# Kernel tuning notes

Hardware: AMD Instinct MI355X
Metric: run time of the kernel (lower is better)

## Reference

```python
import jax, jax.numpy as jnp
import numpy as np

EMBED_DIM = 1024
ATTN_DIM = 1024


def setup_inputs() -> dict:
    key = jax.random.key(0)
    k1, k2, k3, k4 = jax.random.split(key, 4)
    scale = 1.0 / np.sqrt(EMBED_DIM)
    return {
        "embedded": jax.random.normal(k1, (4, 2048, EMBED_DIM), dtype=jnp.float32),
        # weights stored as [in, out] (torch Linear applies x @ W.T)
        "Wk": jax.random.uniform(k2, (EMBED_DIM, ATTN_DIM), dtype=jnp.float32, minval=-scale, maxval=scale),
        "Wq": jax.random.uniform(k3, (EMBED_DIM, ATTN_DIM), dtype=jnp.float32, minval=-scale, maxval=scale),
        "Wv": jax.random.uniform(k4, (EMBED_DIM, ATTN_DIM), dtype=jnp.float32, minval=-scale, maxval=scale),
    }


def reference(embedded, Wk, Wq, Wv):
    b, t, _ = embedded.shape
    k = embedded @ Wk  # [b, t, d]
    q = embedded @ Wq
    v = embedded @ Wv
    scores = jnp.einsum("btd,bsd->bts", q, k) / jnp.sqrt(jnp.float32(k.shape[-1]))
    causal = jnp.tril(jnp.ones((t, t), dtype=bool))  # [t, t]
    scores = jnp.where(causal, scores, -jnp.inf)
    w = jax.nn.softmax(scores, axis=-1)
    o = jnp.einsum("bts,bsd->btd", w, v)
    return jnp.round(o * 10000.0) / 10000.0
```

## Files before the change

### kernel.cpp

```cpp
#include <hip/hip_runtime.h>
#include <cmath>

typedef _Float16 half8 __attribute__((ext_vector_type(8)));
typedef _Float16 half4 __attribute__((ext_vector_type(4)));
typedef float floatx4 __attribute__((ext_vector_type(4)));

__device__ __forceinline__ void load_lds16(const void* g, void* l) {
  __builtin_amdgcn_global_load_lds((const __attribute__((address_space(1))) void*)g,
                                   (__attribute__((address_space(3))) void*)l, 16, 0, 0);
}

__device__ __forceinline__ unsigned lds_addr(const void* p) {
  return (unsigned)(unsigned long long)(const __attribute__((address_space(3))) void*)p;
}

__device__ __forceinline__ half8 ds_read128(unsigned addr) {
  half8 r;
  asm volatile("ds_read_b128 %0, %1" : "=v"(r) : "v"(addr));
  return r;
}


__global__ void prep_kernel(const float* __restrict__ emb, const float* __restrict__ Wq,
                            const float* __restrict__ Wk, const float* __restrict__ Wv,
                            _Float16* __restrict__ Xp, _Float16* __restrict__ Wqp,
                            _Float16* __restrict__ Wkp, _Float16* __restrict__ Wvtp) {
  int p = blockIdx.x;
  if (p < 640) {
    __shared__ _Float16 lds[16 * 1032];
    const float* src;
    _Float16* dst;
    if (p < 512)      { src = emb + (size_t)p * 16384;        dst = Xp  + (size_t)p * 16384; }
    else if (p < 576) { src = Wq + (size_t)(p - 512) * 16384; dst = Wqp + (size_t)(p - 512) * 16384; }
    else              { src = Wk + (size_t)(p - 576) * 16384; dst = Wkp + (size_t)(p - 576) * 16384; }
    for (int it = 0; it < 16; ++it) {
      int idx = it * 256 + threadIdx.x;
      int row = idx >> 8, c4 = idx & 255;
      float4 v = ((const float4*)src)[row * 256 + c4];
      half4 h;
      h[0] = (_Float16)v.x; h[1] = (_Float16)v.y; h[2] = (_Float16)v.z; h[3] = (_Float16)v.w;
      *(half4*)(lds + row * 1032 + c4 * 4) = h;
    }
    __syncthreads();
    for (int it = 0; it < 8; ++it) {
      int c = it * 256 + threadIdx.x;
      int kb = c >> 6, k16 = (c >> 4) & 3, r = c & 15;
      half8 h = *(const half8*)(lds + r * 1032 + kb * 32 + k16 * 8);
      *(half8*)(dst + (size_t)c * 8) = h;
    }
  } else {
    __shared__ float tile[32][33];
    int q = p - 640;
    int n0 = (q & 31) * 32, k0 = (q >> 5) * 32;
    int c = threadIdx.x & 31, r8 = threadIdx.x >> 5;
    for (int pp = 0; pp < 4; ++pp) {
      int r = pp * 8 + r8;
      tile[r][c] = Wv[(size_t)(k0 + r) * 1024 + n0 + c];
    }
    __syncthreads();
    if (threadIdx.x < 128) {
      int rr = threadIdx.x & 31;
      int k16 = (threadIdx.x >> 5) & 3;
      half8 h;
      for (int kk = 0; kk < 8; ++kk) h[kk] = (_Float16)tile[k16 * 8 + kk][rr];
      int n_row = n0 + rr;
      size_t chunk = ((size_t)(n_row >> 4) * 32 + (k0 >> 5)) * 64 + (k16 << 4) + (n_row & 15);
      *(half8*)(Wvtp + chunk * 8) = h;
    }
  }
}

__device__ __forceinline__ void gemm_core(const _Float16* __restrict__ Ap, int kbA, int tA0,
                                          const _Float16* __restrict__ Bp, int kbB, int tB0,
                                          int kIters, _Float16* sA, _Float16* sB,
                                          floatx4 acc[4][4]) {
  int tid = threadIdx.x;
  int lane = tid & 63, wave = tid >> 6;
  int wm = (wave >> 1) << 6, wn = (wave & 1) << 6;
  const _Float16* gA0 = Ap + ((size_t)(tA0 + 2 * wave) * kbA) * 512 + lane * 8;
  const _Float16* gA1 = Ap + ((size_t)(tA0 + 2 * wave + 1) * kbA) * 512 + lane * 8;
  const _Float16* gB0 = Bp + ((size_t)(tB0 + 2 * wave) * kbB) * 512 + lane * 8;
  const _Float16* gB1 = Bp + ((size_t)(tB0 + 2 * wave + 1) * kbB) * 512 + lane * 8;
  int ta = wm >> 4, tb = wn >> 4, lo = lane * 8;
  int wo = wave * 1024;

  load_lds16(gA0, sA + wo);
  load_lds16(gA1, sA + wo + 512);
  load_lds16(gB0, sB + wo);
  load_lds16(gB1, sB + wo + 512);
  __syncthreads();

  int cur = 0;
  for (int kt = 0; kt < kIters; ++kt) {
    if (kt + 1 < kIters) {
      size_t kb = (size_t)(kt + 1) * 512;
      int nx = (cur ^ 1) << 12;
      load_lds16(gA0 + kb, sA + nx + wo);
      load_lds16(gA1 + kb, sA + nx + wo + 512);
      load_lds16(gB0 + kb, sB + nx + wo);
      load_lds16(gB1 + kb, sB + nx + wo + 512);
    }
    const _Float16* cA = sA + (cur << 12);
    const _Float16* cB = sB + (cur << 12);
    half8 af[4], bf[4];
    for (int i = 0; i < 4; ++i) af[i] = *(const half8*)(cA + (ta + i) * 512 + lo);
    for (int j = 0; j < 4; ++j) bf[j] = *(const half8*)(cB + (tb + j) * 512 + lo);
    __builtin_amdgcn_s_setprio(1);
    for (int i = 0; i < 4; ++i)
      for (int j = 0; j < 4; ++j)
        acc[i][j] = __builtin_amdgcn_mfma_f32_16x16x32_f16(af[i], bf[j], acc[i][j], 0, 0, 0);
    __builtin_amdgcn_s_setprio(0);
    if (kt + 1 < kIters) {
      __syncthreads();
      cur ^= 1;
    }
  }
}

__global__ void mt_kernel(const _Float16* __restrict__ Wkp, const _Float16* __restrict__ Wqp,
                          _Float16* __restrict__ Mtp) {
  __shared__ __align__(16) _Float16 sA[8192];
  __shared__ __align__(16) _Float16 sB[8192];
  floatx4 acc[4][4];
  for (int i = 0; i < 4; ++i)
    for (int j = 0; j < 4; ++j) acc[i][j] = (floatx4){0.f, 0.f, 0.f, 0.f};
  int m0 = blockIdx.y * 128, n0 = blockIdx.x * 128;
  gemm_core(Wkp, 32, m0 >> 4, Wqp, 32, n0 >> 4, 32, sA, sB, acc);
  int lane = threadIdx.x & 63, wave = threadIdx.x >> 6;
  int wm = (wave >> 1) << 6, wn = (wave & 1) << 6;
  int quad = lane >> 4, cl = lane & 15;
  for (int i = 0; i < 4; ++i)
    for (int j = 0; j < 4; ++j)
      for (int rr = 0; rr < 4; ++rr) {
        int row = m0 + wm + i * 16 + quad * 4 + rr;
        int col = n0 + wn + j * 16 + cl;
        size_t chunk = ((size_t)(row >> 4) * 32 + (col >> 5)) * 64 + (((col >> 3) & 3) << 4) + (row & 15);
        Mtp[chunk * 8 + (col & 7)] = (_Float16)acc[i][j][rr];
      }
}

#define NT_PROJ 16

__global__ __launch_bounds__(512, 2) void proj256_kernel(
    const _Float16* __restrict__ Ap, const _Float16* __restrict__ Bp,
    _Float16* __restrict__ XMp, _Float16* __restrict__ Vtp) {
  __shared__ __align__(16) _Float16 sh[65536];
  int tid = threadIdx.x;
  int lane = tid & 63, w = tid >> 6;
  int wr = w >> 2, wc = w & 3;
  int orig = blockIdx.x;
  int tile = (orig & 7) * 32 + (orig >> 3);
  int mtile = tile >> 3, ntile = tile & 7;
  int tA0 = mtile * 16, tB0 = ntile * 16;

  const _Float16* gB[4];
  int ldsB[4];
  for (int i = 0; i < 4; ++i) {
    int cb = w * 4 + i, pc = cb >> 1, kb = cb & 1;
    gB[i] = Bp + ((size_t)(tB0 + pc) * 32 + kb) * 512 + lane * 8;
    ldsB[i] = 16384 + cb * 512;
  }
  const _Float16* gA[4];
  int ldsA[4];
  {
    int kbw = w & 1, pihi = (w >> 2) * 8, pilo = (w >> 1) & 1;
    for (int q = 0; q < 4; ++q) {
      int p = 2 * q + pilo + pihi;
      gA[q] = Ap + ((size_t)(tA0 + p) * 32 + kbw) * 512 + lane * 8;
      ldsA[q] = (p * 2 + kbw) * 512;
    }
  }

  unsigned L = lds_addr(sh);
  unsigned baseA = L + (unsigned)(wr * 16384 + lane * 16);
  unsigned baseB = L + 32768u + (unsigned)(wc * 8192 + lane * 16);

  floatx4 acc[8][4];
  for (int m = 0; m < 8; ++m)
    for (int n = 0; n < 4; ++n) acc[m][n] = (floatx4){0.f, 0.f, 0.f, 0.f};

  for (int tt = 0; tt < 2; ++tt) {
    int bo = tt << 15;
    for (int i = 0; i < 4; ++i) load_lds16(gB[i] + (size_t)tt * 1024, sh + bo + ldsB[i]);
    for (int q = 0; q < 4; ++q) load_lds16(gA[q] + (size_t)tt * 1024, sh + bo + ldsA[q]);
  }
  asm volatile("s_waitcnt vmcnt(8)" ::: "memory");
  __builtin_amdgcn_s_barrier();

  half8 bf[4][2];
#pragma unroll 2
  for (int t = 0; t < NT_PROJ; ++t) {
    int bo = (t & 1) << 15;
    unsigned bob = (unsigned)(t & 1) << 16;
    unsigned aA = baseA + bob, aB = baseB + bob;
#pragma unroll
    for (int q = 0; q < 4; ++q) {
      half8 af[2][2];
      if (q == 0) {
        for (int n = 0; n < 4; ++n)
          for (int kb = 0; kb < 2; ++kb)
            bf[n][kb] = ds_read128(aB + (unsigned)(n * 2048 + kb * 1024));
      }
      for (int mm = 0; mm < 2; ++mm)
        for (int kb = 0; kb < 2; ++kb)
          af[mm][kb] = ds_read128(aA + (unsigned)((2 * q + mm) * 2048 + kb * 1024));
      if (q == 0) {
        if (t >= 1 && t + 1 < NT_PROJ)
          load_lds16(gA[3] + (size_t)(t + 1) * 1024, sh + (bo ^ 32768) + ldsA[3]);
      } else if (q == 1) {
        if (t + 2 < NT_PROJ)
          for (int i = 0; i < 4; ++i)
            load_lds16(gB[i] + (size_t)(t + 2) * 1024, sh + bo + ldsB[i]);
      } else if (q == 2) {
        if (t + 2 < NT_PROJ) {
          load_lds16(gA[0] + (size_t)(t + 2) * 1024, sh + bo + ldsA[0]);
          load_lds16(gA[1] + (size_t)(t + 2) * 1024, sh + bo + ldsA[1]);
        }
      } else {
        if (t < NT_PROJ - 1) {
          if (t + 2 < NT_PROJ) asm volatile("s_waitcnt vmcnt(6)" ::: "memory");
          else                 asm volatile("s_waitcnt vmcnt(0)" ::: "memory");
        }
        if (t + 2 < NT_PROJ)
          load_lds16(gA[2] + (size_t)(t + 2) * 1024, sh + bo + ldsA[2]);
      }
      __builtin_amdgcn_s_barrier();
      asm volatile("s_waitcnt lgkmcnt(0)" ::: "memory");
      __builtin_amdgcn_sched_barrier(0);
      __builtin_amdgcn_s_setprio(1);
      for (int mm = 0; mm < 2; ++mm)
        for (int n = 0; n < 4; ++n)
          for (int kb = 0; kb < 2; ++kb)
            acc[2 * q + mm][n] =
                __builtin_amdgcn_mfma_f32_16x16x32_f16(af[mm][kb], bf[n][kb], acc[2 * q + mm][n], 0, 0, 0);
      __builtin_amdgcn_s_setprio(0);
      __builtin_amdgcn_sched_barrier(0);
      __builtin_amdgcn_s_barrier();
    }
  }

  int quad = lane >> 4, cl = lane & 15;
  int which = ntile >> 2;
  for (int m = 0; m < 8; ++m)
    for (int n = 0; n < 4; ++n)
      for (int rr = 0; rr < 4; ++rr) {
        int rl = wr * 128 + m * 16 + quad * 4 + rr;
        int cg = wc * 64 + n * 16 + cl;
        _Float16 val = (_Float16)acc[m][n][rr];
        int lh;
        if (which) {
          lh = (((cg >> 4) * 8 + (rl >> 5)) << 9) + (((rl >> 3) & 3) << 7) + ((cg & 15) << 3) + (rl & 7);
        } else {
          lh = (((rl >> 4) * 8 + (cg >> 5)) << 9) + (((cg >> 3) & 3) << 7) + ((rl & 15) << 3) + (cg & 7);
        }
        sh[lh] = val;
      }
  __syncthreads();
  int b = mtile >> 3;
  if (which) {
    _Float16* dst = Vtp + (size_t)b * 2097152;
    for (int p = 0; p < 16; ++p) {
      size_t GB = (((size_t)(ntile & 3) * 16 + p) * 64 + (mtile & 7) * 8) * 512;
      *(half8*)(dst + GB + tid * 8) = *(const half8*)(sh + p * 4096 + tid * 8);
    }
  } else {
    _Float16* dst = XMp + (size_t)b * 2097152;
    for (int p = 0; p < 16; ++p) {
      size_t GB = (((size_t)(mtile & 7) * 16 + p) * 32 + (ntile & 3) * 8) * 512;
      *(half8*)(dst + GB + tid * 8) = *(const half8*)(sh + p * 4096 + tid * 8);
    }
  }
}

__global__ void qke_kernel(const _Float16* __restrict__ XMp, const _Float16* __restrict__ Xp,
                           _Float16* __restrict__ E, float* __restrict__ lsum) {
  __shared__ __align__(16) _Float16 sh[16384];
  int x = blockIdx.x, b = blockIdx.y;
  int p = (x & 7) * 17 + (x >> 3);
  int ti = 0;
  while ((ti + 1) * (ti + 2) / 2 <= p) ++ti;
  int tj = p - ti * (ti + 1) / 2;
  const _Float16* Ab = XMp + (size_t)b * 2097152;
  const _Float16* Bb = Xp + (size_t)b * 2097152;
  _Float16* Eb = E + (size_t)b * 4194304;
  floatx4 acc[4][4];
  for (int i = 0; i < 4; ++i)
    for (int j = 0; j < 4; ++j) acc[i][j] = (floatx4){0.f, 0.f, 0.f, 0.f};
  gemm_core(Ab, 32, ti * 8, Bb, 32, tj * 8, 32, sh, sh + 8192, acc);
  int lane = threadIdx.x & 63, wave = threadIdx.x >> 6;
  int wm = (wave >> 1) << 6, wn = (wave & 1) << 6;
  int quad = lane >> 4, cl = lane & 15;
  float rs[4][4];
  for (int i = 0; i < 4; ++i)
    for (int rr = 0; rr < 4; ++rr) rs[i][rr] = 0.f;
  __syncthreads();
  for (int i = 0; i < 4; ++i)
    for (int j = 0; j < 4; ++j)
      for (int rr = 0; rr < 4; ++rr) {
        int rl = wm + i * 16 + quad * 4 + rr;
        int cg = wn + j * 16 + cl;
        int row = ti * 128 + rl, col = tj * 128 + cg;
        float e = 0.f;
        if (col <= row) e = __expf(acc[i][j][rr] * 0.03125f - 12.0f);
        _Float16 eh = (_Float16)e;
        rs[i][rr] += (float)eh;
        int lh = (((rl >> 4) * 4 + (cg >> 5)) << 9) + (((cg >> 3) & 3) << 7) + ((rl & 15) << 3) + (cg & 7);
        sh[lh] = eh;
      }
  __syncthreads();
  for (int pp = 0; pp < 8; ++pp) {
    size_t GB = ((size_t)(ti * 8 + pp) * 64 + tj * 4) * 512;
    *(half8*)(Eb + GB + threadIdx.x * 8) = *(const half8*)(sh + pp * 2048 + threadIdx.x * 8);
  }
  float* lb = lsum + (size_t)b * 2048;
  for (int i = 0; i < 4; ++i)
    for (int rr = 0; rr < 4; ++rr) {
      float v = rs[i][rr];
      v += __shfl_xor(v, 1, 64);
      v += __shfl_xor(v, 2, 64);
      v += __shfl_xor(v, 4, 64);
      v += __shfl_xor(v, 8, 64);
      if (cl == 0) atomicAdd(lb + ti * 128 + wm + i * 16 + quad * 4 + rr, v);
    }
}

__global__ void pv_kernel(const _Float16* __restrict__ E, const _Float16* __restrict__ Vtp,
                          const float* __restrict__ lsum, float* __restrict__ out) {
  __shared__ __align__(16) _Float16 sA[8192];
  __shared__ __align__(16) _Float16 sB[8192];
  int orig = blockIdx.x + 8 * (blockIdx.y + 16 * blockIdx.z);
  int logical = (orig & 7) * 64 + (orig >> 3);
  int n0 = (logical & 7) * 128;
  int rest = logical >> 3;
  int y = rest & 15, b = rest >> 4;
  int ti = (y & 1) ? (15 - (y >> 1)) : (y >> 1);
  const _Float16* Pb = E + (size_t)b * 4194304;
  const _Float16* Vb = Vtp + (size_t)b * 2097152;
  floatx4 acc[4][4];
  for (int i = 0; i < 4; ++i)
    for (int j = 0; j < 4; ++j) acc[i][j] = (floatx4){0.f, 0.f, 0.f, 0.f};
  gemm_core(Pb, 64, ti * 8, Vb, 64, n0 >> 4, (ti + 1) * 4, sA, sB, acc);
  int lane = threadIdx.x & 63, wave = threadIdx.x >> 6;
  int wm = (wave >> 1) << 6, wn = (wave & 1) << 6;
  int quad = lane >> 4, cl = lane & 15;
  const float* lb = lsum + (size_t)b * 2048;
  for (int i = 0; i < 4; ++i)
    for (int rr = 0; rr < 4; ++rr) {
      int row = ti * 128 + wm + i * 16 + quad * 4 + rr;
      float inv = 1.0f / lb[row];
      for (int j = 0; j < 4; ++j) {
        int col = n0 + wn + j * 16 + cl;
        float v = acc[i][j][rr] * inv;
        out[((size_t)b * 2048 + row) * 1024 + col] = rintf(v * 10000.f) * 1e-4f;
      }
    }
}

extern "C" void kernel_launch(void* const* d_in, const int* in_sizes, int n_in,
                              void* d_out, int out_size, void* d_ws, size_t ws_size,
                              hipStream_t stream) {
  const float* emb = (const float*)d_in[0];
  const float* Wk = (const float*)d_in[1];
  const float* Wq = (const float*)d_in[2];
  const float* Wv = (const float*)d_in[3];
  float* out = (float*)d_out;

  _Float16* ws = (_Float16*)d_ws;
  _Float16* Xp   = ws;
  _Float16* Wqp  = Xp + (size_t)8192 * 1024;
  _Float16* Wkp  = Wqp + (size_t)1024 * 1024;
  _Float16* Mtp  = Wkp + (size_t)1024 * 1024;
  _Float16* Wvtp = Mtp + (size_t)1024 * 1024;
  _Float16* XMp  = Wvtp + (size_t)1024 * 1024;
  _Float16* Vtp  = XMp + (size_t)8192 * 1024;
  _Float16* Ebuf = Vtp + (size_t)8192 * 1024;
  float* lsum    = (float*)(Ebuf + (size_t)16 * 1024 * 1024);

  hipMemsetAsync(lsum, 0, 4 * 2048 * sizeof(float), stream);
  prep_kernel<<<1664, 256, 0, stream>>>(emb, Wq, Wk, Wv, Xp, Wqp, Wkp, Wvtp);
  mt_kernel<<<dim3(8, 8), 256, 0, stream>>>(Wkp, Wqp, Mtp);
  proj256_kernel<<<256, 512, 0, stream>>>(Xp, Mtp, XMp, Vtp);
  qke_kernel<<<dim3(136, 4), 256, 0, stream>>>(XMp, Xp, Ebuf, lsum);
  pv_kernel<<<dim3(8, 16, 4), 256, 0, stream>>>(Ebuf, Vtp, lsum, out);
}
```

Measured before the change: 223.3 us.

## Swizzle projection epilogue LDS, drop a barrier, vectorize PV output stores

```diff
diff --git a/kernel.cpp b/kernel.cpp
--- a/kernel.cpp
+++ b/kernel.cpp
@@ -18,6 +18,10 @@
   half8 r;
   asm volatile("ds_read_b128 %0, %1" : "=v"(r) : "v"(addr));
   return r;
+}
+
+__device__ __forceinline__ unsigned mswz(unsigned a) {
+  return a ^ (((a >> 7) & 1u) << 3) ^ (((a >> 6) & 1u) << 4);
 }
 
 
@@ -224,7 +228,6 @@
         if (t + 2 < NT_PROJ)
           load_lds16(gA[2] + (size_t)(t + 2) * 1024, sh + bo + ldsA[2]);
       }
-      __builtin_amdgcn_s_barrier();
       asm volatile("s_waitcnt lgkmcnt(0)" ::: "memory");
       __builtin_amdgcn_sched_barrier(0);
       __builtin_amdgcn_s_setprio(1);
@@ -247,13 +250,13 @@
         int rl = wr * 128 + m * 16 + quad * 4 + rr;
         int cg = wc * 64 + n * 16 + cl;
         _Float16 val = (_Float16)acc[m][n][rr];
-        int lh;
+        unsigned lh;
         if (which) {
-          lh = (((cg >> 4) * 8 + (rl >> 5)) << 9) + (((rl >> 3) & 3) << 7) + ((cg & 15) << 3) + (rl & 7);
+          lh = (((unsigned)(cg >> 4) * 8 + (rl >> 5)) << 9) + (((rl >> 3) & 3) << 7) + ((cg & 15) << 3) + (rl & 7);
         } else {
-          lh = (((rl >> 4) * 8 + (cg >> 5)) << 9) + (((cg >> 3) & 3) << 7) + ((rl & 15) << 3) + (cg & 7);
+          lh = (((unsigned)(rl >> 4) * 8 + (cg >> 5)) << 9) + (((cg >> 3) & 3) << 7) + ((rl & 15) << 3) + (cg & 7);
         }
-        sh[lh] = val;
+        sh[mswz(lh)] = val;
       }
   __syncthreads();
   int b = mtile >> 3;
@@ -261,13 +264,13 @@
     _Float16* dst = Vtp + (size_t)b * 2097152;
     for (int p = 0; p < 16; ++p) {
       size_t GB = (((size_t)(ntile & 3) * 16 + p) * 64 + (mtile & 7) * 8) * 512;
-      *(half8*)(dst + GB + tid * 8) = *(const half8*)(sh + p * 4096 + tid * 8);
+      *(half8*)(dst + GB + tid * 8) = *(const half8*)(sh + mswz((unsigned)(p * 4096 + tid * 8)));
     }
   } else {
     _Float16* dst = XMp + (size_t)b * 2097152;
     for (int p = 0; p < 16; ++p) {
       size_t GB = (((size_t)(mtile & 7) * 16 + p) * 32 + (ntile & 3) * 8) * 512;
-      *(half8*)(dst + GB + tid * 8) = *(const half8*)(sh + p * 4096 + tid * 8);
+      *(half8*)(dst + GB + tid * 8) = *(const half8*)(sh + mswz((unsigned)(p * 4096 + tid * 8)));
     }
   }
 }
@@ -339,21 +342,25 @@
   floatx4 acc[4][4];
   for (int i = 0; i < 4; ++i)
     for (int j = 0; j < 4; ++j) acc[i][j] = (floatx4){0.f, 0.f, 0.f, 0.f};
-  gemm_core(Pb, 64, ti * 8, Vb, 64, n0 >> 4, (ti + 1) * 4, sA, sB, acc);
+  gemm_core(Vb, 64, n0 >> 4, Pb, 64, ti * 8, (ti + 1) * 4, sA, sB, acc);
   int lane = threadIdx.x & 63, wave = threadIdx.x >> 6;
   int wm = (wave >> 1) << 6, wn = (wave & 1) << 6;
   int quad = lane >> 4, cl = lane & 15;
   const float* lb = lsum + (size_t)b * 2048;
-  for (int i = 0; i < 4; ++i)
-    for (int rr = 0; rr < 4; ++rr) {
-      int row = ti * 128 + wm + i * 16 + quad * 4 + rr;
-      float inv = 1.0f / lb[row];
-      for (int j = 0; j < 4; ++j) {
-        int col = n0 + wn + j * 16 + cl;
-        float v = acc[i][j][rr] * inv;
-        out[((size_t)b * 2048 + row) * 1024 + col] = rintf(v * 10000.f) * 1e-4f;
-      }
-    }
+  for (int j = 0; j < 4; ++j) {
+    int t = ti * 128 + wn + j * 16 + cl;
+    float inv = 1.0f / lb[t];
+    float* orow = out + ((size_t)b * 2048 + t) * 1024;
+    for (int i = 0; i < 4; ++i) {
+      int d0 = n0 + wm + i * 16 + quad * 4;
+      float4 v;
+      v.x = rintf(acc[i][j][0] * inv * 10000.f) * 1e-4f;
+      v.y = rintf(acc[i][j][1] * inv * 10000.f) * 1e-4f;
+      v.z = rintf(acc[i][j][2] * inv * 10000.f) * 1e-4f;
+      v.w = rintf(acc[i][j][3] * inv * 10000.f) * 1e-4f;
+      *(float4*)(orow + d0) = v;
+    }
+  }
 }
 
 extern "C" void kernel_launch(void* const* d_in, const int* in_sizes, int n_in,
```

Measured after the change: 259.2 us. +16.0%, slower.
